# Performance work log

Hardware: AMD Instinct MI355X
Metric: run time of the kernel (lower is better)

The kernel has to match this reference:

```python
import jax, jax.numpy as jnp
import numpy as np

B, C, HS, WS = 2, 256, 64, 64
NH, DK, DV = 2, 128, 128
EPS = 1e-6


def setup_inputs() -> dict:
    key = jax.random.key(0)
    ks = jax.random.split(key, 8)
    s = 0.02
    return {
        "x": jax.random.normal(ks[0], (B, C, HS, WS), jnp.float32),
        "Wq": jax.random.normal(ks[1], (NH, DK, C), jnp.float32) * s,
        "bq": jnp.zeros((NH, DK), jnp.float32),
        "Wk": jax.random.normal(ks[2], (NH, DK, C), jnp.float32) * s,
        "bk": jnp.zeros((NH, DK), jnp.float32),
        "Wv": jax.random.normal(ks[3], (NH, DV, C), jnp.float32) * s,
        "bv": jnp.zeros((NH, DV), jnp.float32),
        "scale": jnp.ones((NH,), jnp.float32),  # softmax_scale per head (l2scaled)
        "Wm": jax.random.normal(ks[4], (C, NH * DV), jnp.float32) * s,
        "bm": jnp.zeros((C,), jnp.float32),
    }


def _l2norm(t):
    # F.normalize along channel dim (axis=2 of [B,H,dk,L]) with eps=1e-6
    n = jnp.sqrt(jnp.sum(t * t, axis=2, keepdims=True))
    return t / jnp.maximum(n, EPS)


def reference(x, Wq, bq, Wk, bk, Wv, bv, scale, Wm, bm):
    b, c, h, w = x.shape
    L = h * w
    xf = x.reshape(b, c, L)                               # [B,C,L]
    # 1x1 conv QKV projections (per head)
    Q = jnp.einsum('hkc,bcl->bhkl', Wq, xf) + bq[None, :, :, None]
    K = jnp.einsum('hkc,bcl->bhkl', Wk, xf) + bk[None, :, :, None]
    V = jnp.einsum('hvc,bcl->bhvl', Wv, xf) + bv[None, :, :, None]
    # l2scaled QK-normalization: cosine similarity with learned scale
    sc = jnp.sqrt(scale)[None, :, None, None]             # scale**0.5 per head
    Qn = _l2norm(Q) * sc
    Kn = _l2norm(K) * sc
    # attention over spatial tokens: [B,H,L,L]
    A = jax.nn.softmax(jnp.einsum('bhkl,bhkm->bhlm', Qn, Kn), axis=-1)
    R = jnp.einsum('bhlm,bhvm->bhvl', A, V)               # [B,H,dv,L]
    R = R.reshape(b, NH * DV, L)                          # concat heads on channels
    out = jnp.einsum('oc,bcl->bol', Wm, R) + bm[None, :, None]  # 1x1 merge conv
    out = out.reshape(b, c, h, w)
    return out + x                                        # residual (nnd op is identity)
```

## Files before the change

kernel.cpp:

```cpp
#include <hip/hip_runtime.h>


#define BB  2
#define CC  256
#define LL  4096
#define NHD 2
#define DKD 128
#define DVD 128

#define QBLK   64
#define KVBLK  64
#define SPLITK 2
#define TPS    (LL / SPLITK / KVBLK)

typedef short  short8  __attribute__((ext_vector_type(8)));
typedef float  f32x4   __attribute__((ext_vector_type(4)));
typedef unsigned short ushort4v __attribute__((ext_vector_type(4)));

__device__ __forceinline__ unsigned short f2bf(float f) {
  union { float f; unsigned u; } v; v.f = f;
  unsigned r = v.u + 0x7fffu + ((v.u >> 16) & 1u);
  return (unsigned short)(r >> 16);
}
__device__ __forceinline__ float bf2f(unsigned short u) {
  union { unsigned u; float f; } v; v.u = ((unsigned)u) << 16;
  return v.f;
}
__device__ __forceinline__ void glds16(const unsigned short* g, unsigned short* l) {
  __builtin_amdgcn_global_load_lds(
      (const __attribute__((address_space(1))) void*)g,
      (__attribute__((address_space(3))) void*)l, 16, 0, 0);
}

__global__ __launch_bounds__(256) void mhsa_pre_kernel(
    const float* __restrict__ x,
    const float* __restrict__ Wq, const float* __restrict__ Wk,
    const float* __restrict__ Wv, const float* __restrict__ Wm,
    unsigned short* __restrict__ Xt, unsigned short* __restrict__ wbf,
    unsigned short* __restrict__ wmb)
{
  const int z = blockIdx.z;
  if (z == 2) {
    if (blockIdx.y) return;
    int base = blockIdx.x * 2048 + threadIdx.x;
    #pragma unroll
    for (int i = 0; i < 8; ++i) {
      int idx = base + i * 256;
      if (idx < 196608) {
        int p = idx >> 16;
        int rem = idx & 65535;
        const float* W = p == 0 ? Wq : (p == 1 ? Wk : Wv);
        wbf[idx] = f2bf(W[rem]);
      } else {
        wmb[idx - 196608] = f2bf(Wm[idx - 196608]);
      }
    }
    return;
  }
  const int b  = z;
  const int l0 = blockIdx.x * 32, c0 = blockIdx.y * 32;
  __shared__ float Ts[32][33];
  const int tid = threadIdx.x;
  const int tl  = tid & 31, tc = tid >> 5;
  const float* xb = x + (size_t)b * CC * LL;
  #pragma unroll
  for (int pp = 0; pp < 4; ++pp) {
    int c = tc + pp * 8;
    Ts[c][tl] = xb[(size_t)(c0 + c) * LL + l0 + tl];
  }
  __syncthreads();
  unsigned short* Xb = Xt + (size_t)b * LL * CC;
  #pragma unroll
  for (int pp = 0; pp < 4; ++pp) {
    int l = tc + pp * 8;
    Xb[(size_t)(l0 + l) * CC + c0 + tl] = f2bf(Ts[tl][l]);
  }
}

__global__ __launch_bounds__(256) void mhsa_projm_kernel(
    const unsigned short* __restrict__ Xt,
    const unsigned short* __restrict__ wbf,
    const float* __restrict__ bq, const float* __restrict__ bk,
    const float* __restrict__ bv, const float* __restrict__ scale,
    unsigned short* __restrict__ qn, unsigned short* __restrict__ kn,
    unsigned short* __restrict__ vb)
{
  const int lt0 = blockIdx.x * 64;
  const int bh  = blockIdx.y;
  const int p   = blockIdx.z;
  const int h   = bh & 1, b = bh >> 1;

  const unsigned short* W = wbf + ((size_t)p * 2 + h) * (128 * 256);
  const unsigned short* X = Xt + (size_t)b * LL * CC;
  const float* bias = (p == 0 ? bq : (p == 1 ? bk : bv)) + h * 128;

  __shared__ unsigned short Ws[2][128 * 64];
  __shared__ unsigned short Xs[2][64 * 64];
  __shared__ float red[4][64];

  const int wave = threadIdx.x >> 6;
  const int lane = threadIdx.x & 63;
  const int lr = lane & 15, lc = lane >> 4;

  int offW[4], ldsW[4], offX[2], ldsX[2];
  #pragma unroll
  for (int j = 0; j < 4; ++j) {
    int ii = wave * 4 + j;
    int r  = ii * 8 + (lane >> 3);
    int c  = (lane & 7) ^ (lane >> 3);
    offW[j] = r * 256 + c * 8;
    ldsW[j] = ii * 512;
  }
  #pragma unroll
  for (int j = 0; j < 2; ++j) {
    int ii = wave * 2 + j;
    int r  = ii * 8 + (lane >> 3);
    int c  = (lane & 7) ^ (lane >> 3);
    offX[j] = (lt0 + r) * 256 + c * 8;
    ldsX[j] = ii * 512;
  }

  f32x4 acc[2][4];
  #pragma unroll
  for (int kt2 = 0; kt2 < 2; ++kt2)
    #pragma unroll
    for (int lt = 0; lt < 4; ++lt) acc[kt2][lt] = (f32x4){0.f, 0.f, 0.f, 0.f};

  #pragma unroll
  for (int j = 0; j < 4; ++j) glds16(W + offW[j], &Ws[0][ldsW[j]]);
  #pragma unroll
  for (int j = 0; j < 2; ++j) glds16(X + offX[j], &Xs[0][ldsX[j]]);
  __syncthreads();

  const int sw = lr & 7;
  int buf = 0;
  for (int step = 0; step < 4; ++step) {
    if (step < 3) {
      int c0 = (step + 1) * 64;
      #pragma unroll
      for (int j = 0; j < 4; ++j) glds16(W + c0 + offW[j], &Ws[buf ^ 1][ldsW[j]]);
      #pragma unroll
      for (int j = 0; j < 2; ++j) glds16(X + c0 + offX[j], &Xs[buf ^ 1][ldsX[j]]);
    }
    #pragma unroll
    for (int ks = 0; ks < 2; ++ks) {
      short8 af[2], bf_[4];
      #pragma unroll
      for (int kt2 = 0; kt2 < 2; ++kt2)
        af[kt2] = *reinterpret_cast<const short8*>(
            &Ws[buf][(wave * 32 + kt2 * 16 + lr) * 64 + ((ks * 4 + lc) ^ sw) * 8]);
      #pragma unroll
      for (int lt = 0; lt < 4; ++lt)
        bf_[lt] = *reinterpret_cast<const short8*>(
            &Xs[buf][(lt * 16 + lr) * 64 + ((ks * 4 + lc) ^ sw) * 8]);
      #pragma unroll
      for (int kt2 = 0; kt2 < 2; ++kt2)
        #pragma unroll
        for (int lt = 0; lt < 4; ++lt)
          acc[kt2][lt] = __builtin_amdgcn_mfma_f32_16x16x32_bf16(
              af[kt2], bf_[lt], acc[kt2][lt], 0, 0, 0);
    }
    __syncthreads();
    buf ^= 1;
  }

  #pragma unroll
  for (int kt2 = 0; kt2 < 2; ++kt2)
    #pragma unroll
    for (int r = 0; r < 4; ++r) {
      float bsv = bias[wave * 32 + kt2 * 16 + lc * 4 + r];
      #pragma unroll
      for (int lt = 0; lt < 4; ++lt) acc[kt2][lt][r] += bsv;
    }

  if (p < 2) {
    float s[4];
    #pragma unroll
    for (int lt = 0; lt < 4; ++lt) {
      float v = 0.f;
      #pragma unroll
      for (int kt2 = 0; kt2 < 2; ++kt2)
        #pragma unroll
        for (int r = 0; r < 4; ++r) v += acc[kt2][lt][r] * acc[kt2][lt][r];
      v += __shfl_xor(v, 16, 64);
      v += __shfl_xor(v, 32, 64);
      s[lt] = v;
    }
    if (lc == 0) {
      #pragma unroll
      for (int lt = 0; lt < 4; ++lt) red[wave][lt * 16 + lr] = s[lt];
    }
    __syncthreads();
    float sq = sqrtf(scale[h]);
    unsigned short* out = (p == 0 ? qn : kn) + (size_t)bh * LL * DKD;
    #pragma unroll
    for (int lt = 0; lt < 4; ++lt) {
      int l = lt * 16 + lr;
      float sum = red[0][l] + red[1][l] + red[2][l] + red[3][l];
      float nv = sq / fmaxf(sqrtf(sum), 1e-6f);
      #pragma unroll
      for (int kt2 = 0; kt2 < 2; ++kt2) {
        ushort4v pk;
        #pragma unroll
        for (int r = 0; r < 4; ++r) pk[r] = f2bf(acc[kt2][lt][r] * nv);
        *reinterpret_cast<ushort4v*>(
            out + (size_t)(lt0 + l) * DKD + wave * 32 + kt2 * 16 + lc * 4) = pk;
      }
    }
  } else {
    unsigned short* outv = vb + (size_t)bh * DVD * LL;
    #pragma unroll
    for (int kt2 = 0; kt2 < 2; ++kt2)
      #pragma unroll
      for (int r = 0; r < 4; ++r)
        #pragma unroll
        for (int lt = 0; lt < 4; ++lt)
          outv[(size_t)(wave * 32 + kt2 * 16 + lc * 4 + r) * LL + lt0 + lt * 16 + lr]
              = f2bf(acc[kt2][lt][r]);
  }
}

__global__ __launch_bounds__(256) void mhsa_attn_kernel(
    const unsigned short* __restrict__ qn,
    const unsigned short* __restrict__ kn,
    const unsigned short* __restrict__ vb,
    const float* __restrict__ scale,
    unsigned short* __restrict__ pr,
    float* __restrict__ ls)
{
  const int wgid = (blockIdx.z * gridDim.y + blockIdx.y) * gridDim.x + blockIdx.x;
  const int xcd  = wgid & 7;
  const int slot = wgid >> 3;
  const int bh   = xcd >> 1;
  const int qt   = ((xcd & 1) << 5) | (slot & 31);
  const int s    = slot >> 5;
  const int l0   = qt * QBLK;
  const int kbase = s * (LL / SPLITK);

  const int wave = threadIdx.x >> 6;
  const int lane = threadIdx.x & 63;
  const int lr   = lane & 15;
  const int lc   = lane >> 4;

  const unsigned short* Q = qn + (size_t)bh * LL * DKD;
  const unsigned short* K = kn + (size_t)bh * LL * DKD;
  const unsigned short* V = vb + (size_t)bh * DVD * LL;
  const float M = scale[bh & 1];

  __shared__ unsigned short Ks[2][KVBLK * DKD];
  __shared__ unsigned short Vs[2][DVD * KVBLK];
  __shared__ unsigned short plds[4][16 * 72];
  unsigned short* myp = plds[wave];

  const int l0w = l0 + wave * 16;
  short8 qf[4];
  #pragma unroll
  for (int ks = 0; ks < 4; ++ks)
    qf[ks] = *reinterpret_cast<const short8*>(Q + (size_t)(l0w + lr) * DKD + ks * 32 + lc * 8);

  int offK[4], offV[4], ldsOff[4];
  #pragma unroll
  for (int j = 0; j < 4; ++j) {
    int ii = wave * 4 + j;
    int rK = ii * 4 + (lane >> 4);
    int cK = (lane & 15) ^ (rK & 7);
    offK[j] = rK * DKD + cK * 8;
    int vV = ii * 8 + (lane >> 3);
    int cV = (lane & 7) ^ (lane >> 3);
    offV[j] = vV * LL + cV * 8;
    ldsOff[j] = ii * 512;
  }

  f32x4 racc[8];
  #pragma unroll
  for (int vt = 0; vt < 8; ++vt) racc[vt] = (f32x4){0.f, 0.f, 0.f, 0.f};
  float lsum[4] = {0.f, 0.f, 0.f, 0.f};

  #pragma unroll
  for (int j = 0; j < 4; ++j) {
    glds16(K + (size_t)kbase * DKD + offK[j], &Ks[0][ldsOff[j]]);
    glds16(V + kbase + offV[j],               &Vs[0][ldsOff[j]]);
  }
  __syncthreads();

  const int sw = lr & 7;
  int buf = 0;
  for (int t = 0; t < TPS; ++t) {
    if (t + 1 < TPS) {
      int m1 = kbase + (t + 1) * KVBLK;
      #pragma unroll
      for (int j = 0; j < 4; ++j) {
        glds16(K + (size_t)m1 * DKD + offK[j], &Ks[buf ^ 1][ldsOff[j]]);
        glds16(V + m1 + offV[j],               &Vs[buf ^ 1][ldsOff[j]]);
      }
    }

    f32x4 sx[4];
    #pragma unroll
    for (int ct = 0; ct < 4; ++ct) {
      f32x4 acc = (f32x4){0.f, 0.f, 0.f, 0.f};
      #pragma unroll
      for (int ks = 0; ks < 4; ++ks) {
        short8 kf = *reinterpret_cast<const short8*>(
            &Ks[buf][(ct * 16 + lr) * DKD + ((ks * 4 + lc) ^ sw) * 8]);
        acc = __builtin_amdgcn_mfma_f32_16x16x32_bf16(qf[ks], kf, acc, 0, 0, 0);
      }
      sx[ct] = acc;
    }

    #pragma unroll
    for (int ct = 0; ct < 4; ++ct) {
      #pragma unroll
      for (int r = 0; r < 4; ++r) {
        float pv = __expf(sx[ct][r] - M);
        sx[ct][r] = pv;
        lsum[r] += pv;
      }
    }

    #pragma unroll
    for (int ct = 0; ct < 4; ++ct)
      #pragma unroll
      for (int r = 0; r < 4; ++r)
        myp[(lc * 4 + r) * 72 + ct * 16 + lr] = f2bf(sx[ct][r]);

    short8 pf[2];
    #pragma unroll
    for (int ks = 0; ks < 2; ++ks)
      pf[ks] = *reinterpret_cast<const short8*>(&myp[lr * 72 + ks * 32 + lc * 8]);

    #pragma unroll
    for (int vt = 0; vt < 8; ++vt) {
      #pragma unroll
      for (int ks = 0; ks < 2; ++ks) {
        short8 vf = *reinterpret_cast<const short8*>(
            &Vs[buf][(vt * 16 + lr) * KVBLK + ((ks * 4 + lc) ^ sw) * 8]);
        racc[vt] = __builtin_amdgcn_mfma_f32_16x16x32_bf16(pf[ks], vf, racc[vt], 0, 0, 0);
      }
    }

    __syncthreads();
    buf ^= 1;
  }

  #pragma unroll
  for (int r = 0; r < 4; ++r) {
    float v = lsum[r];
    #pragma unroll
    for (int msk = 8; msk; msk >>= 1) v += __shfl_xor(v, msk, 64);
    lsum[r] = v;
  }
  if (lr == 0) {
    #pragma unroll
    for (int r = 0; r < 4; ++r)
      ls[((size_t)s * 4 + bh) * LL + l0w + lc * 4 + r] = lsum[r];
  }

  unsigned short* Pb = pr + ((size_t)s * 4 + bh) * DVD * LL;
  #pragma unroll
  for (int vt = 0; vt < 8; ++vt) {
    ushort4v pk;
    #pragma unroll
    for (int r = 0; r < 4; ++r) pk[r] = f2bf(racc[vt][r]);
    *reinterpret_cast<ushort4v*>(Pb + (size_t)(vt * 16 + lr) * LL + l0w + lc * 4) = pk;
  }
}

__global__ __launch_bounds__(256) void mhsa_combine_kernel(
    const unsigned short* __restrict__ pr,
    const float* __restrict__ ls,
    unsigned short* __restrict__ Rt)
{
  const int l0 = blockIdx.x * 32;
  const int c0 = blockIdx.y * 32;
  const int b  = blockIdx.z;
  const int hh = c0 >> 7;

  __shared__ float Ts[32][33];
  __shared__ float invl[32];

  const int tid = threadIdx.x;
  const int tl  = tid & 31, tc = tid >> 5;

  if (tid < 32) {
    size_t bhl = (size_t)(b * NHD + hh) * LL + l0 + tid;
    invl[tid] = 1.f / (ls[bhl] + ls[(size_t)4 * LL + bhl]);
  }
  __syncthreads();

  const size_t sstride = (size_t)4 * DVD * LL;
  #pragma unroll
  for (int pp = 0; pp < 4; ++pp) {
    int cl = tc + pp * 8;
    int v  = (c0 & 127) + cl;
    size_t idx = ((size_t)(b * NHD + hh) * DVD + v) * LL + l0 + tl;
    Ts[cl][tl] = (bf2f(pr[idx]) + bf2f(pr[sstride + idx])) * invl[tl];
  }
  __syncthreads();

  unsigned short* Rb = Rt + (size_t)b * LL * CC;
  #pragma unroll
  for (int pp = 0; pp < 4; ++pp) {
    int ll = tc + pp * 8;
    Rb[(size_t)(l0 + ll) * CC + c0 + tl] = f2bf(Ts[tl][ll]);
  }
}

__global__ __launch_bounds__(256) void mhsa_mergem_kernel(
    const unsigned short* __restrict__ Rt,
    const unsigned short* __restrict__ wmb,
    const float* __restrict__ bm,
    const float* __restrict__ x,
    float* __restrict__ out)
{
  const int lt0 = blockIdx.x * 64;
  const int oh  = blockIdx.y;
  const int b   = blockIdx.z;

  const unsigned short* W = wmb + (size_t)oh * 128 * 256;
  const unsigned short* X = Rt + (size_t)b * LL * CC;

  __shared__ unsigned short Ws[2][128 * 64];
  __shared__ unsigned short Xs[2][64 * 64];

  const int wave = threadIdx.x >> 6;
  const int lane = threadIdx.x & 63;
  const int lr = lane & 15, lc = lane >> 4;

  int offW[4], ldsW[4], offX[2], ldsX[2];
  #pragma unroll
  for (int j = 0; j < 4; ++j) {
    int ii = wave * 4 + j;
    int r  = ii * 8 + (lane >> 3);
    int c  = (lane & 7) ^ (lane >> 3);
    offW[j] = r * 256 + c * 8;
    ldsW[j] = ii * 512;
  }
  #pragma unroll
  for (int j = 0; j < 2; ++j) {
    int ii = wave * 2 + j;
    int r  = ii * 8 + (lane >> 3);
    int c  = (lane & 7) ^ (lane >> 3);
    offX[j] = (lt0 + r) * 256 + c * 8;
    ldsX[j] = ii * 512;
  }

  f32x4 acc[2][4];
  #pragma unroll
  for (int kt2 = 0; kt2 < 2; ++kt2)
    #pragma unroll
    for (int lt = 0; lt < 4; ++lt) acc[kt2][lt] = (f32x4){0.f, 0.f, 0.f, 0.f};

  #pragma unroll
  for (int j = 0; j < 4; ++j) glds16(W + offW[j], &Ws[0][ldsW[j]]);
  #pragma unroll
  for (int j = 0; j < 2; ++j) glds16(X + offX[j], &Xs[0][ldsX[j]]);
  __syncthreads();

  const int sw = lr & 7;
  int buf = 0;
  for (int step = 0; step < 4; ++step) {
    if (step < 3) {
      int c0 = (step + 1) * 64;
      #pragma unroll
      for (int j = 0; j < 4; ++j) glds16(W + c0 + offW[j], &Ws[buf ^ 1][ldsW[j]]);
      #pragma unroll
      for (int j = 0; j < 2; ++j) glds16(X + c0 + offX[j], &Xs[buf ^ 1][ldsX[j]]);
    }
    #pragma unroll
    for (int ks = 0; ks < 2; ++ks) {
      short8 af[2], bf_[4];
      #pragma unroll
      for (int kt2 = 0; kt2 < 2; ++kt2)
        af[kt2] = *reinterpret_cast<const short8*>(
            &Ws[buf][(wave * 32 + kt2 * 16 + lr) * 64 + ((ks * 4 + lc) ^ sw) * 8]);
      #pragma unroll
      for (int lt = 0; lt < 4; ++lt)
        bf_[lt] = *reinterpret_cast<const short8*>(
            &Xs[buf][(lt * 16 + lr) * 64 + ((ks * 4 + lc) ^ sw) * 8]);
      #pragma unroll
      for (int kt2 = 0; kt2 < 2; ++kt2)
        #pragma unroll
        for (int lt = 0; lt < 4; ++lt)
          acc[kt2][lt] = __builtin_amdgcn_mfma_f32_16x16x32_bf16(
              af[kt2], bf_[lt], acc[kt2][lt], 0, 0, 0);
    }
    __syncthreads();
    buf ^= 1;
  }

  #pragma unroll
  for (int kt2 = 0; kt2 < 2; ++kt2) {
    #pragma unroll
    for (int r = 0; r < 4; ++r) {
      int o = oh * 128 + wave * 32 + kt2 * 16 + lc * 4 + r;
      float bias = bm[o];
      #pragma unroll
      for (int lt = 0; lt < 4; ++lt) {
        size_t off = ((size_t)(b * CC + o)) * LL + lt0 + lt * 16 + lr;
        out[off] = acc[kt2][lt][r] + bias + x[off];
      }
    }
  }
}

extern "C" void kernel_launch(void* const* d_in, const int* in_sizes, int n_in,
                              void* d_out, int out_size, void* d_ws, size_t ws_size,
                              hipStream_t stream) {
  const float* x     = (const float*)d_in[0];
  const float* Wq    = (const float*)d_in[1];
  const float* bq    = (const float*)d_in[2];
  const float* Wk    = (const float*)d_in[3];
  const float* bk    = (const float*)d_in[4];
  const float* Wv    = (const float*)d_in[5];
  const float* bv    = (const float*)d_in[6];
  const float* scale = (const float*)d_in[7];
  const float* Wm    = (const float*)d_in[8];
  const float* bm    = (const float*)d_in[9];
  float* out = (float*)d_out;

  const size_t nqk = (size_t)BB * NHD * LL * DKD;
  const size_t npr = (size_t)SPLITK * BB * NHD * DVD * LL;
  unsigned short* qn = (unsigned short*)d_ws;
  unsigned short* kn = qn + nqk;
  unsigned short* vb = kn + nqk;
  unsigned short* pr = vb + nqk;
  float* lsw = (float*)(pr + npr);
  unsigned short* wmb = (unsigned short*)(lsw + (size_t)SPLITK * BB * NHD * LL);
  unsigned short* Xt  = pr;
  unsigned short* wbf = pr + (size_t)BB * LL * CC;
  unsigned short* Rt  = qn;

  mhsa_pre_kernel<<<dim3(128, 8, 3), dim3(256), 0, stream>>>(
      x, Wq, Wk, Wv, Wm, Xt, wbf, wmb);
  mhsa_projm_kernel<<<dim3(LL / 64, BB * NHD, 3), dim3(256), 0, stream>>>(
      Xt, wbf, bq, bk, bv, scale, qn, kn, vb);
  mhsa_attn_kernel<<<dim3(LL / QBLK, BB * NHD, SPLITK), dim3(256), 0, stream>>>(
      qn, kn, vb, scale, pr, lsw);
  mhsa_combine_kernel<<<dim3(LL / 32, CC / 32, BB), dim3(256), 0, stream>>>(
      pr, lsw, Rt);
  mhsa_mergem_kernel<<<dim3(LL / 64, 2, BB), dim3(256), 0, stream>>>(
      Rt, wmb, bm, x, out);
}
```

Measured before the change: 95.49 us.

## Split attention KV range four ways with smaller KV tiles when workspace allows

The attention kernel now takes a runtime KV chunk size and the grid's z dimension becomes a split count chosen on the host (4 if the workspace is large enough, otherwise 2). The KV tile shrinks from 64 to 32 rows, with matching changes to the LDS swizzle, load mapping and P staging, which halves shared memory per block. The aim is more workgroups and higher occupancy to fill the GPU's CUs. In exchange, the combine kernel must read and sum more partial planes, which adds memory traffic, and the smaller tiles mean more loop iterations and barriers per block.

```diff
diff --git a/kernel.cpp b/kernel.cpp
--- a/kernel.cpp
+++ b/kernel.cpp
@@ -9,9 +9,7 @@
 #define DVD 128
 
 #define QBLK   64
-#define KVBLK  64
-#define SPLITK 2
-#define TPS    (LL / SPLITK / KVBLK)
+#define KVBLK  32
 
 typedef short  short8  __attribute__((ext_vector_type(8)));
 typedef float  f32x4   __attribute__((ext_vector_type(4)));
@@ -226,7 +224,8 @@
     const unsigned short* __restrict__ vb,
     const float* __restrict__ scale,
     unsigned short* __restrict__ pr,
-    float* __restrict__ ls)
+    float* __restrict__ ls,
+    int kchunk)
 {
   const int wgid = (blockIdx.z * gridDim.y + blockIdx.y) * gridDim.x + blockIdx.x;
   const int xcd  = wgid & 7;
@@ -235,7 +234,8 @@
   const int qt   = ((xcd & 1) << 5) | (slot & 31);
   const int s    = slot >> 5;
   const int l0   = qt * QBLK;
-  const int kbase = s * (LL / SPLITK);
+  const int kbase = s * kchunk;
+  const int tps  = kchunk / KVBLK;
 
   const int wave = threadIdx.x >> 6;
   const int lane = threadIdx.x & 63;
@@ -249,7 +249,7 @@
 
   __shared__ unsigned short Ks[2][KVBLK * DKD];
   __shared__ unsigned short Vs[2][DVD * KVBLK];
-  __shared__ unsigned short plds[4][16 * 72];
+  __shared__ unsigned short plds[4][16 * 40];
   unsigned short* myp = plds[wave];
 
   const int l0w = l0 + wave * 16;
@@ -258,15 +258,15 @@
   for (int ks = 0; ks < 4; ++ks)
     qf[ks] = *reinterpret_cast<const short8*>(Q + (size_t)(l0w + lr) * DKD + ks * 32 + lc * 8);
 
-  int offK[4], offV[4], ldsOff[4];
-  #pragma unroll
-  for (int j = 0; j < 4; ++j) {
-    int ii = wave * 4 + j;
+  int offK[2], offV[2], ldsOff[2];
+  #pragma unroll
+  for (int j = 0; j < 2; ++j) {
+    int ii = wave * 2 + j;
     int rK = ii * 4 + (lane >> 4);
     int cK = (lane & 15) ^ (rK & 7);
     offK[j] = rK * DKD + cK * 8;
-    int vV = ii * 8 + (lane >> 3);
-    int cV = (lane & 7) ^ (lane >> 3);
+    int vV = ii * 16 + (lane >> 2);
+    int cV = (lane & 3) ^ ((vV >> 1) & 3);
     offV[j] = vV * LL + cV * 8;
     ldsOff[j] = ii * 512;
   }
@@ -277,27 +277,28 @@
   float lsum[4] = {0.f, 0.f, 0.f, 0.f};
 
   #pragma unroll
-  for (int j = 0; j < 4; ++j) {
+  for (int j = 0; j < 2; ++j) {
     glds16(K + (size_t)kbase * DKD + offK[j], &Ks[0][ldsOff[j]]);
     glds16(V + kbase + offV[j],               &Vs[0][ldsOff[j]]);
   }
   __syncthreads();
 
-  const int sw = lr & 7;
+  const int sw  = lr & 7;
+  const int swV = (lr >> 1) & 3;
   int buf = 0;
-  for (int t = 0; t < TPS; ++t) {
-    if (t + 1 < TPS) {
+  for (int t = 0; t < tps; ++t) {
+    if (t + 1 < tps) {
       int m1 = kbase + (t + 1) * KVBLK;
       #pragma unroll
-      for (int j = 0; j < 4; ++j) {
+      for (int j = 0; j < 2; ++j) {
         glds16(K + (size_t)m1 * DKD + offK[j], &Ks[buf ^ 1][ldsOff[j]]);
         glds16(V + m1 + offV[j],               &Vs[buf ^ 1][ldsOff[j]]);
       }
     }
 
-    f32x4 sx[4];
-    #pragma unroll
-    for (int ct = 0; ct < 4; ++ct) {
+    f32x4 sx[2];
+    #pragma unroll
+    for (int ct = 0; ct < 2; ++ct) {
       f32x4 acc = (f32x4){0.f, 0.f, 0.f, 0.f};
       #pragma unroll
       for (int ks = 0; ks < 4; ++ks) {
@@ -309,7 +310,7 @@
     }
 
     #pragma unroll
-    for (int ct = 0; ct < 4; ++ct) {
+    for (int ct = 0; ct < 2; ++ct) {
       #pragma unroll
       for (int r = 0; r < 4; ++r) {
         float pv = __expf(sx[ct][r] - M);
@@ -319,24 +320,18 @@
     }
 
     #pragma unroll
-    for (int ct = 0; ct < 4; ++ct)
+    for (int ct = 0; ct < 2; ++ct)
       #pragma unroll
       for (int r = 0; r < 4; ++r)
-        myp[(lc * 4 + r) * 72 + ct * 16 + lr] = f2bf(sx[ct][r]);
-
-    short8 pf[2];
-    #pragma unroll
-    for (int ks = 0; ks < 2; ++ks)
-      pf[ks] = *reinterpret_cast<const short8*>(&myp[lr * 72 + ks * 32 + lc * 8]);
+        myp[(lc * 4 + r) * 40 + ct * 16 + lr] = f2bf(sx[ct][r]);
+
+    short8 pf = *reinterpret_cast<const short8*>(&myp[lr * 40 + lc * 8]);
 
     #pragma unroll
     for (int vt = 0; vt < 8; ++vt) {
-      #pragma unroll
-      for (int ks = 0; ks < 2; ++ks) {
-        short8 vf = *reinterpret_cast<const short8*>(
-            &Vs[buf][(vt * 16 + lr) * KVBLK + ((ks * 4 + lc) ^ sw) * 8]);
-        racc[vt] = __builtin_amdgcn_mfma_f32_16x16x32_bf16(pf[ks], vf, racc[vt], 0, 0, 0);
-      }
+      short8 vf = *reinterpret_cast<const short8*>(
+          &Vs[buf][(vt * 16 + lr) * KVBLK + (lc ^ swV) * 8]);
+      racc[vt] = __builtin_amdgcn_mfma_f32_16x16x32_bf16(pf, vf, racc[vt], 0, 0, 0);
     }
 
     __syncthreads();
@@ -369,7 +364,8 @@
 __global__ __launch_bounds__(256) void mhsa_combine_kernel(
     const unsigned short* __restrict__ pr,
     const float* __restrict__ ls,
-    unsigned short* __restrict__ Rt)
+    unsigned short* __restrict__ Rt,
+    int ns)
 {
   const int l0 = blockIdx.x * 32;
   const int c0 = blockIdx.y * 32;
@@ -384,7 +380,9 @@
 
   if (tid < 32) {
     size_t bhl = (size_t)(b * NHD + hh) * LL + l0 + tid;
-    invl[tid] = 1.f / (ls[bhl] + ls[(size_t)4 * LL + bhl]);
+    float t = 0.f;
+    for (int s = 0; s < ns; ++s) t += ls[bhl + (size_t)s * 4 * LL];
+    invl[tid] = 1.f / t;
   }
   __syncthreads();
 
@@ -394,7 +392,9 @@
     int cl = tc + pp * 8;
     int v  = (c0 & 127) + cl;
     size_t idx = ((size_t)(b * NHD + hh) * DVD + v) * LL + l0 + tl;
-    Ts[cl][tl] = (bf2f(pr[idx]) + bf2f(pr[sstride + idx])) * invl[tl];
+    float a = 0.f;
+    for (int s = 0; s < ns; ++s) a += bf2f(pr[idx + (size_t)s * sstride]);
+    Ts[cl][tl] = a * invl[tl];
   }
   __syncthreads();
 
@@ -519,14 +519,20 @@
   const float* bm    = (const float*)d_in[9];
   float* out = (float*)d_out;
 
-  const size_t nqk = (size_t)BB * NHD * LL * DKD;
-  const size_t npr = (size_t)SPLITK * BB * NHD * DVD * LL;
+  const size_t nqk    = (size_t)BB * NHD * LL * DKD;
+  const size_t prPlane = (size_t)BB * NHD * DVD * LL;
+  const size_t lsPlane = (size_t)BB * NHD * LL;
+
+  size_t need4 = 3 * nqk * 2 + 4 * prPlane * 2 + 4 * lsPlane * 4 + 65536 * 2;
+  const int ns = (ws_size >= need4) ? 4 : 2;
+  const int kchunk = LL / ns;
+
   unsigned short* qn = (unsigned short*)d_ws;
   unsigned short* kn = qn + nqk;
   unsigned short* vb = kn + nqk;
   unsigned short* pr = vb + nqk;
-  float* lsw = (float*)(pr + npr);
-  unsigned short* wmb = (unsigned short*)(lsw + (size_t)SPLITK * BB * NHD * LL);
+  float* lsw = (float*)(pr + (size_t)ns * prPlane);
+  unsigned short* wmb = (unsigned short*)(lsw + (size_t)ns * lsPlane);
   unsigned short* Xt  = pr;
   unsigned short* wbf = pr + (size_t)BB * LL * CC;
   unsigned short* Rt  = qn;
@@ -535,10 +541,10 @@
       x, Wq, Wk, Wv, Wm, Xt, wbf, wmb);
   mhsa_projm_kernel<<<dim3(LL / 64, BB * NHD, 3), dim3(256), 0, stream>>>(
       Xt, wbf, bq, bk, bv, scale, qn, kn, vb);
-  mhsa_attn_kernel<<<dim3(LL / QBLK, BB * NHD, SPLITK), dim3(256), 0, stream>>>(
-      qn, kn, vb, scale, pr, lsw);
+  mhsa_attn_kernel<<<dim3(LL / QBLK, BB * NHD, ns), dim3(256), 0, stream>>>(
+      qn, kn, vb, scale, pr, lsw, kchunk);
   mhsa_combine_kernel<<<dim3(LL / 32, CC / 32, BB), dim3(256), 0, stream>>>(
-      pr, lsw, Rt);
+      pr, lsw, Rt, ns);
   mhsa_mergem_kernel<<<dim3(LL / 64, 2, BB), dim3(256), 0, stream>>>(
       Rt, wmb, bm, x, out);
 }
```

Result: faster. 90.66 us (-5.1%).
